# Performance work log

Measured on AMD Instinct MI355X. Metric: run time of the kernel, lower is better.

The kernel has to match this reference:

```python
import jax, jax.numpy as jnp
import numpy as np

NUM_HEADS = 16
HEAD_DIM = 64
WINDOW = 512  # attention_window; band half-width = WINDOW // 2
MAX_TIME = 10000.0  # rotary default max timescale


def apply_rotary(x):
    """Rotary encoding as in pos_encs_lib.apply_rotary_encoding.

    x: [b, t, h, d]. Pairs (x[2i], x[2i+1]) are rotated by angle pos * inv_freq,
    with inv_freq repeated per pair (interleaved layout).
    """
    d = x.shape[-1]
    freq_seq = jnp.arange(d // 2, dtype=jnp.float32) / (d // 2)
    inv_freq = jnp.repeat(MAX_TIME ** -freq_seq, 2)  # [d]
    pos = jnp.arange(x.shape[1], dtype=jnp.float32)
    t = pos[None, :, None, None] * inv_freq[None, None, None, :]  # [1,t,1,d]
    xp = x.reshape(*x.shape[:-1], d // 2, 2)
    x_rot = jnp.stack([-xp[..., 1], xp[..., 0]], axis=-1).reshape(x.shape)
    return x * jnp.cos(t).astype(x.dtype) + x_rot * jnp.sin(t).astype(x.dtype)


def setup_inputs() -> dict:
    key = jax.random.key(0)
    ks = jax.random.split(key, 6)
    B, T, E = 4, 2048, 1024
    H = NUM_HEADS * HEAD_DIM
    return {
        "inputs_q": jax.random.normal(ks[0], (B, T, E), jnp.float32),
        "inputs_kv": jax.random.normal(ks[1], (B, T, E), jnp.float32),
        "Wq": jax.random.normal(ks[2], (E, H), jnp.float32) * 0.02,
        "Wk": jax.random.normal(ks[3], (E, H), jnp.float32) * 0.02,
        "Wv": jax.random.normal(ks[4], (E, H), jnp.float32) * 0.02,
        "Wo": jax.random.normal(ks[5], (H, E), jnp.float32) * 0.02,
    }


def reference(inputs_q, inputs_kv, Wq, Wk, Wv, Wo):
    b, T, E = inputs_q.shape
    q = (inputs_q @ Wq).reshape(b, T, NUM_HEADS, HEAD_DIM)
    k = (inputs_kv @ Wk).reshape(b, T, NUM_HEADS, HEAD_DIM)
    v = (inputs_kv @ Wv).reshape(b, T, NUM_HEADS, HEAD_DIM)
    q = apply_rotary(q)
    k = apply_rotary(k)
    # [b, h, t, T] attention logits, scaled by 1/sqrt(head_dim)
    att = jnp.einsum('bthd,bThd->bhtT', q, k) * (1.0 / np.sqrt(HEAD_DIM))
    # sliding-window band mask: |i - j| <= WINDOW // 2 (matches k-diagonal sum)
    idx = jnp.arange(T)
    band = jnp.abs(idx[:, None] - idx[None, :]) <= (WINDOW // 2)
    att = jnp.where(band, att, jnp.finfo(jnp.float32).min)
    p = jax.nn.softmax(att, axis=-1)
    out = jnp.einsum('bhtT,bThd->bthd', p, v).reshape(b, T, NUM_HEADS * HEAD_DIM)
    return out @ Wo
```

## Files before the change

### kernel.cpp

```cpp
#include <hip/hip_runtime.h>
#include <hip/hip_bf16.h>


typedef __attribute__((ext_vector_type(8))) short s8v;
typedef __attribute__((ext_vector_type(4))) float f4v;

#define MFMA_BF16 __builtin_amdgcn_mfma_f32_16x16x32_bf16

#define ASYNC_CP16(g, l)                                             \
  __builtin_amdgcn_global_load_lds(                                  \
      (const __attribute__((address_space(1))) void*)(g),            \
      (__attribute__((address_space(3))) void*)(l), 16, 0, 0)

#define SWZ(row, g) ((row) * 64 + ((((g) ^ ((row) & 7))) * 8))

__device__ __forceinline__ unsigned short f2bf(float f) {
  union { float f; unsigned int u; } v; v.f = f;
  unsigned int r = (v.u + 0x7fffu + ((v.u >> 16) & 1u)) >> 16;
  return (unsigned short)r;
}

__device__ __forceinline__ unsigned int pack_bf16(float a, float b) {
  union { __hip_bfloat162 h; unsigned int u; } cv;
  cv.h = __float22bfloat162_rn(make_float2(a, b));
  return cv.u;
}

__global__ __launch_bounds__(256) void cvt2_kernel(
    const float* __restrict__ s0, const float* __restrict__ s1,
    unsigned short* __restrict__ d0, unsigned short* __restrict__ d1) {
  int g = blockIdx.x;
  const float* src = (g < 8192) ? s0 : s1;
  unsigned short* dst = (g < 8192) ? d0 : d1;
  int i = ((g & 8191) * 256 + threadIdx.x) * 4;
  float4 v = *(const float4*)(src + i);
  ushort4 o;
  o.x = f2bf(v.x); o.y = f2bf(v.y); o.z = f2bf(v.z); o.w = f2bf(v.w);
  *(ushort4*)(dst + i) = o;
}

__global__ __launch_bounds__(256) void wtrans_kernel(
    const float* __restrict__ W0, const float* __restrict__ W1,
    const float* __restrict__ W2, const float* __restrict__ W3,
    unsigned short* __restrict__ D0, unsigned short* __restrict__ D1,
    unsigned short* __restrict__ D2, unsigned short* __restrict__ D3) {
  const float* W = blockIdx.z == 0 ? W0 : blockIdx.z == 1 ? W1 : blockIdx.z == 2 ? W2 : W3;
  unsigned short* D = blockIdx.z == 0 ? D0 : blockIdx.z == 1 ? D1 : blockIdx.z == 2 ? D2 : D3;
  __shared__ float tile[32][33];
  int n0 = blockIdx.x * 32, k0 = blockIdx.y * 32;
  int tx = threadIdx.x & 31, ty = threadIdx.x >> 5;
#pragma unroll
  for (int r = 0; r < 32; r += 8)
    tile[ty + r][tx] = W[(size_t)(k0 + ty + r) * 1024 + n0 + tx];
  __syncthreads();
#pragma unroll
  for (int r = 0; r < 32; r += 8)
    D[(size_t)(n0 + ty + r) * 1024 + k0 + tx] = f2bf(tile[tx][ty + r]);
}

__global__ __launch_bounds__(256) void proj_gemm(
    const unsigned short* __restrict__ XqBf, const unsigned short* __restrict__ XkvBf,
    const unsigned short* __restrict__ Wtq, const unsigned short* __restrict__ Wtk,
    const unsigned short* __restrict__ Wtv,
    unsigned short* __restrict__ Qb, unsigned short* __restrict__ Kb,
    unsigned short* __restrict__ Vt) {
  const int K = 1024;
  int z = blockIdx.z;
  const unsigned short* A  = (z == 0) ? XqBf : XkvBf;
  const unsigned short* Bt = (z == 0) ? Wtq : (z == 1) ? Wtk : Wtv;

  __shared__ __align__(16) unsigned short sA[128 * 64];
  __shared__ __align__(16) unsigned short sB[128 * 64];

  int tid = threadIdx.x;
  int lane = tid & 63, wave = tid >> 6;
  int quad = lane >> 4, l16 = lane & 15;
  int wm = wave & 1, wn = wave >> 1;
  int m_blk = blockIdx.x * 128, n_blk = blockIdx.y * 128;

  f4v acc[4][4] = {};
  int srow = tid >> 3, sg = (tid & 7) ^ (srow & 7);
  const unsigned short* gA = A + (size_t)(m_blk + srow) * K + sg * 8;
  const unsigned short* gB = Bt + (size_t)(n_blk + srow) * K + sg * 8;

  for (int k0 = 0; k0 < K; k0 += 64) {
#pragma unroll
    for (int i = 0; i < 4; ++i) {
      ASYNC_CP16(gA + (size_t)i * 32 * K + k0, &sA[i * 2048 + tid * 8]);
      ASYNC_CP16(gB + (size_t)i * 32 * K + k0, &sB[i * 2048 + tid * 8]);
    }
    __syncthreads();
#pragma unroll
    for (int ks = 0; ks < 64; ks += 32) {
      s8v af[4], bf[4];
#pragma unroll
      for (int mt = 0; mt < 4; ++mt)
        af[mt] = *(const s8v*)&sA[SWZ(wm * 64 + mt * 16 + l16, quad + (ks >> 3))];
#pragma unroll
      for (int nt = 0; nt < 4; ++nt)
        bf[nt] = *(const s8v*)&sB[SWZ(wn * 64 + nt * 16 + l16, quad + (ks >> 3))];
#pragma unroll
      for (int mt = 0; mt < 4; ++mt)
#pragma unroll
        for (int nt = 0; nt < 4; ++nt)
          acc[mt][nt] = MFMA_BF16(af[mt], bf[nt], acc[mt][nt], 0, 0, 0);
    }
    __syncthreads();
  }

  if (z < 2) {
    unsigned short* Cb = (z == 0) ? Qb : Kb;
    float post = (z == 0) ? 0.125f : 1.0f;
#pragma unroll
    for (int mt = 0; mt < 4; ++mt)
#pragma unroll
      for (int nt = 0; nt < 4; ++nt)
#pragma unroll
        for (int r = 0; r < 4; ++r) {
          int row = m_blk + wm * 64 + mt * 16 + quad * 4 + r;
          int col = n_blk + wn * 64 + nt * 16 + l16;
          float v = acc[mt][nt][r];
          float other = __shfl_xor(v, 1);
          int dh = col & 63;
          int tpos = row & 2047;
          float fi = (float)(dh >> 1) * (1.0f / 32.0f);
          float invf = __expf(-9.210340371976184f * fi);
          float ang = (float)tpos * invf;
          float s, c;
          __sincosf(ang, &s, &c);
          v = (dh & 1) ? (v * c + other * s) : (v * c - other * s);
          Cb[(size_t)row * 1024 + col] = f2bf(v * post);
        }
  } else {
#pragma unroll
    for (int mt = 0; mt < 4; ++mt)
#pragma unroll
      for (int nt = 0; nt < 4; ++nt) {
        int row0 = m_blk + wm * 64 + mt * 16 + quad * 4;
        int col = n_blk + wn * 64 + nt * 16 + l16;
        int bb = row0 >> 11, t = row0 & 2047;
        int hh = col >> 6, dh = col & 63;
        ushort4 pk;
        pk.x = f2bf(acc[mt][nt][0]);
        pk.y = f2bf(acc[mt][nt][1]);
        pk.z = f2bf(acc[mt][nt][2]);
        pk.w = f2bf(acc[mt][nt][3]);
        *(ushort4*)&Vt[(((size_t)bb * 16 + hh) * 64 + dh) * 2048 + t] = pk;
      }
  }
}

__global__ __launch_bounds__(256, 4) void attn_kernel(
    const unsigned short* __restrict__ Qb, const unsigned short* __restrict__ Kb,
    const unsigned short* __restrict__ Vt, unsigned short* __restrict__ Ab) {
  const int T = 2048;
  int t0 = blockIdx.x * 128;
  int h = blockIdx.y, b = blockIdx.z;
  int tid = threadIdx.x, lane = tid & 63, wave = tid >> 6;
  int quad = lane >> 4, l16 = lane & 15;

  __shared__ __align__(16) unsigned short sK[64][72];
  __shared__ __align__(16) unsigned short sV[64][72];
  __shared__ __align__(16) unsigned short sP[4][16][72];

  size_t base = ((size_t)b * T) * 1024 + (size_t)h * 64;
  size_t vbase = ((size_t)b * 16 + h) * 64 * 2048;
  int qlo = t0 + wave * 32;

  s8v bq[2][2];
#pragma unroll
  for (int f = 0; f < 2; ++f) {
    const unsigned short* g = Qb + base + (size_t)(qlo + f * 16 + l16) * 1024;
    bq[f][0] = *(const s8v*)(g + quad * 8);
    bq[f][1] = *(const s8v*)(g + 32 + quad * 8);
  }

  f4v oacc[2][4] = {};
  float mrow[2] = {-1e30f, -1e30f}, lrow[2] = {0.0f, 0.0f};

  int kv_lo = max(0, t0 - 256);
  int kv_hi = min(T, t0 + 128 + 256);
  int ntiles = (kv_hi - kv_lo) >> 6;

  int srow = tid >> 2, sseg = (tid & 3) * 16;
  const unsigned short* gK = Kb + base + (size_t)(kv_lo + srow) * 1024 + sseg;
  const unsigned short* gV = Vt + vbase + (size_t)srow * 2048 + kv_lo + sseg;
  uint4 rk0 = *(const uint4*)gK, rk1 = *(const uint4*)(gK + 8);
  uint4 rv0 = *(const uint4*)gV, rv1 = *(const uint4*)(gV + 8);

  for (int it = 0; it < ntiles; ++it) {
    int kv0 = kv_lo + (it << 6);
    __syncthreads();
    *(uint4*)&sK[srow][sseg] = rk0;
    *(uint4*)&sK[srow][sseg + 8] = rk1;
    *(uint4*)&sV[srow][sseg] = rv0;
    *(uint4*)&sV[srow][sseg + 8] = rv1;
    __syncthreads();
    if (it + 1 < ntiles) {
      const unsigned short* nK = gK + (size_t)(it + 1) * 64 * 1024;
      const unsigned short* nV = gV + (it + 1) * 64;
      rk0 = *(const uint4*)nK; rk1 = *(const uint4*)(nK + 8);
      rv0 = *(const uint4*)nV; rv1 = *(const uint4*)(nV + 8);
    }
    if (kv0 > qlo + 31 + 256 || kv0 + 63 < qlo - 256) continue;

#pragma unroll
    for (int f = 0; f < 2; ++f) {
      int qf = qlo + f * 16;
      int qg = qf + l16;
      f4v sacc[4];
#pragma unroll
      for (int nt = 0; nt < 4; ++nt) {
        s8v ak0 = *(const s8v*)&sK[nt * 16 + l16][quad * 8];
        s8v ak1 = *(const s8v*)&sK[nt * 16 + l16][32 + quad * 8];
        f4v zz = {};
        zz = MFMA_BF16(ak0, bq[f][0], zz, 0, 0, 0);
        sacc[nt] = MFMA_BF16(ak1, bq[f][1], sacc[nt] = zz, 0, 0, 0);
      }
      bool full = (kv0 >= qf - 241) && (kv0 <= qf + 193);
      if (!full) {
#pragma unroll
        for (int nt = 0; nt < 4; ++nt) {
          int kg = kv0 + nt * 16 + quad * 4;
#pragma unroll
          for (int r = 0; r < 4; ++r) {
            int d = qg - (kg + r);
            if (d > 256 || d < -256) sacc[nt][r] = -1e30f;
          }
        }
      }
      float mymax = sacc[0][0];
#pragma unroll
      for (int nt = 0; nt < 4; ++nt)
#pragma unroll
        for (int r = 0; r < 4; ++r) mymax = fmaxf(mymax, sacc[nt][r]);
      mymax = fmaxf(mymax, __shfl_xor(mymax, 16));
      mymax = fmaxf(mymax, __shfl_xor(mymax, 32));

      float mn = fmaxf(mrow[f], mymax);
      float alpha = __expf(mrow[f] - mn);
      mrow[f] = mn;

      float mysum = 0.0f;
#pragma unroll
      for (int nt = 0; nt < 4; ++nt) {
        float e0 = __expf(sacc[nt][0] - mn);
        float e1 = __expf(sacc[nt][1] - mn);
        float e2 = __expf(sacc[nt][2] - mn);
        float e3 = __expf(sacc[nt][3] - mn);
        mysum += (e0 + e1) + (e2 + e3);
        *(uint2*)&sP[wave][l16][nt * 16 + quad * 4] =
            make_uint2(pack_bf16(e0, e1), pack_bf16(e2, e3));
      }
      mysum += __shfl_xor(mysum, 16);
      mysum += __shfl_xor(mysum, 32);
      lrow[f] = lrow[f] * alpha + mysum;

      s8v pb0 = *(const s8v*)&sP[wave][l16][quad * 8];
      s8v pb1 = *(const s8v*)&sP[wave][l16][32 + quad * 8];

#pragma unroll
      for (int dt = 0; dt < 4; ++dt) {
        s8v av0 = *(const s8v*)&sV[dt * 16 + l16][quad * 8];
        s8v av1 = *(const s8v*)&sV[dt * 16 + l16][32 + quad * 8];
        f4v o = oacc[f][dt];
#pragma unroll
        for (int r = 0; r < 4; ++r) o[r] *= alpha;
        o = MFMA_BF16(av0, pb0, o, 0, 0, 0);
        oacc[f][dt] = MFMA_BF16(av1, pb1, o, 0, 0, 0);
      }
    }
  }

#pragma unroll
  for (int f = 0; f < 2; ++f) {
    float inv = 1.0f / lrow[f];
    size_t rowoff = base + (size_t)(qlo + f * 16 + l16) * 1024;
#pragma unroll
    for (int dt = 0; dt < 4; ++dt) {
      float o0 = oacc[f][dt][0] * inv, o1 = oacc[f][dt][1] * inv;
      float o2 = oacc[f][dt][2] * inv, o3 = oacc[f][dt][3] * inv;
      *(uint2*)&Ab[rowoff + dt * 16 + quad * 4] =
          make_uint2(pack_bf16(o0, o1), pack_bf16(o2, o3));
    }
  }
}

__global__ __launch_bounds__(256) void out_gemm(
    const unsigned short* __restrict__ A, const unsigned short* __restrict__ Bt,
    float* __restrict__ C) {
  const int K = 1024;
  __shared__ __align__(16) unsigned short sA[128 * 64];
  __shared__ __align__(16) unsigned short sB[128 * 64];

  int tid = threadIdx.x;
  int lane = tid & 63, wave = tid >> 6;
  int quad = lane >> 4, l16 = lane & 15;
  int wm = wave & 1, wn = wave >> 1;
  int m_blk = blockIdx.x * 128, n_blk = blockIdx.y * 128;

  f4v acc[4][4] = {};
  int srow = tid >> 3, sg = (tid & 7) ^ (srow & 7);
  const unsigned short* gA = A + (size_t)(m_blk + srow) * K + sg * 8;
  const unsigned short* gB = Bt + (size_t)(n_blk + srow) * K + sg * 8;

  for (int k0 = 0; k0 < K; k0 += 64) {
#pragma unroll
    for (int i = 0; i < 4; ++i) {
      ASYNC_CP16(gA + (size_t)i * 32 * K + k0, &sA[i * 2048 + tid * 8]);
      ASYNC_CP16(gB + (size_t)i * 32 * K + k0, &sB[i * 2048 + tid * 8]);
    }
    __syncthreads();
#pragma unroll
    for (int ks = 0; ks < 64; ks += 32) {
      s8v af[4], bf[4];
#pragma unroll
      for (int mt = 0; mt < 4; ++mt)
        af[mt] = *(const s8v*)&sA[SWZ(wm * 64 + mt * 16 + l16, quad + (ks >> 3))];
#pragma unroll
      for (int nt = 0; nt < 4; ++nt)
        bf[nt] = *(const s8v*)&sB[SWZ(wn * 64 + nt * 16 + l16, quad + (ks >> 3))];
#pragma unroll
      for (int mt = 0; mt < 4; ++mt)
#pragma unroll
        for (int nt = 0; nt < 4; ++nt)
          acc[mt][nt] = MFMA_BF16(af[mt], bf[nt], acc[mt][nt], 0, 0, 0);
    }
    __syncthreads();
  }

#pragma unroll
  for (int mt = 0; mt < 4; ++mt)
#pragma unroll
    for (int nt = 0; nt < 4; ++nt)
#pragma unroll
      for (int r = 0; r < 4; ++r) {
        int row = m_blk + wm * 64 + mt * 16 + quad * 4 + r;
        int col = n_blk + wn * 64 + nt * 16 + l16;
        C[(size_t)row * 1024 + col] = acc[mt][nt][r];
      }
}

extern "C" void kernel_launch(void* const* d_in, const int* in_sizes, int n_in,
                              void* d_out, int out_size, void* d_ws, size_t ws_size,
                              hipStream_t stream) {
  const float* Xq  = (const float*)d_in[0];
  const float* Xkv = (const float*)d_in[1];
  const float* Wq  = (const float*)d_in[2];
  const float* Wk  = (const float*)d_in[3];
  const float* Wv  = (const float*)d_in[4];
  const float* Wo  = (const float*)d_in[5];
  float* out = (float*)d_out;

  char* ws = (char*)d_ws;
  const size_t MB = 1ull << 20;
  unsigned short* XqBf  = (unsigned short*)(ws + 0 * MB);
  unsigned short* XkvBf = (unsigned short*)(ws + 16 * MB);
  unsigned short* Wtq   = (unsigned short*)(ws + 32 * MB);
  unsigned short* Wtk   = (unsigned short*)(ws + 34 * MB);
  unsigned short* Wtv   = (unsigned short*)(ws + 36 * MB);
  unsigned short* Wto   = (unsigned short*)(ws + 38 * MB);
  unsigned short* Qb    = (unsigned short*)(ws + 40 * MB);
  unsigned short* Kb    = (unsigned short*)(ws + 56 * MB);
  unsigned short* Vt    = (unsigned short*)(ws + 72 * MB);
  unsigned short* Ab    = XqBf;

  cvt2_kernel<<<16384, 256, 0, stream>>>(Xq, Xkv, XqBf, XkvBf);
  wtrans_kernel<<<dim3(32, 32, 4), 256, 0, stream>>>(Wq, Wk, Wv, Wo, Wtq, Wtk, Wtv, Wto);
  proj_gemm<<<dim3(64, 8, 3), 256, 0, stream>>>(XqBf, XkvBf, Wtq, Wtk, Wtv, Qb, Kb, Vt);
  attn_kernel<<<dim3(16, 16, 4), 256, 0, stream>>>(Qb, Kb, Vt, Ab);
  out_gemm<<<dim3(64, 8), 256, 0, stream>>>(Ab, Wto, out);
}
```

Measured before the change: 259.0 us.

## Merge prep kernels, fuse K/V projections sharing A tile, enlarge attention blocks

Merges the activation conversion and weight transpose into one prep launch. The projection GEMM now computes K and V in the same block, so the shared inputs_kv tile is loaded once and reused for two accumulator sets. The attention kernel now uses 512-thread blocks covering 256 queries, which amortises K/V tile loads over more queries but lowers occupancy. The K/V GEMM blocks do twice the work, which creates load imbalance against the Q blocks and raises register pressure.

```diff
diff --git a/kernel.cpp b/kernel.cpp
--- a/kernel.cpp
+++ b/kernel.cpp
@@ -26,36 +26,39 @@
   return cv.u;
 }
 
-__global__ __launch_bounds__(256) void cvt2_kernel(
+__global__ __launch_bounds__(256) void prep_kernel(
     const float* __restrict__ s0, const float* __restrict__ s1,
-    unsigned short* __restrict__ d0, unsigned short* __restrict__ d1) {
-  int g = blockIdx.x;
-  const float* src = (g < 8192) ? s0 : s1;
-  unsigned short* dst = (g < 8192) ? d0 : d1;
-  int i = ((g & 8191) * 256 + threadIdx.x) * 4;
-  float4 v = *(const float4*)(src + i);
-  ushort4 o;
-  o.x = f2bf(v.x); o.y = f2bf(v.y); o.z = f2bf(v.z); o.w = f2bf(v.w);
-  *(ushort4*)(dst + i) = o;
-}
-
-__global__ __launch_bounds__(256) void wtrans_kernel(
+    unsigned short* __restrict__ d0, unsigned short* __restrict__ d1,
     const float* __restrict__ W0, const float* __restrict__ W1,
     const float* __restrict__ W2, const float* __restrict__ W3,
     unsigned short* __restrict__ D0, unsigned short* __restrict__ D1,
     unsigned short* __restrict__ D2, unsigned short* __restrict__ D3) {
-  const float* W = blockIdx.z == 0 ? W0 : blockIdx.z == 1 ? W1 : blockIdx.z == 2 ? W2 : W3;
-  unsigned short* D = blockIdx.z == 0 ? D0 : blockIdx.z == 1 ? D1 : blockIdx.z == 2 ? D2 : D3;
-  __shared__ float tile[32][33];
-  int n0 = blockIdx.x * 32, k0 = blockIdx.y * 32;
-  int tx = threadIdx.x & 31, ty = threadIdx.x >> 5;
-#pragma unroll
-  for (int r = 0; r < 32; r += 8)
-    tile[ty + r][tx] = W[(size_t)(k0 + ty + r) * 1024 + n0 + tx];
-  __syncthreads();
-#pragma unroll
-  for (int r = 0; r < 32; r += 8)
-    D[(size_t)(n0 + ty + r) * 1024 + k0 + tx] = f2bf(tile[tx][ty + r]);
+  int g = blockIdx.x;
+  if (g < 16384) {
+    const float* src = (g < 8192) ? s0 : s1;
+    unsigned short* dst = (g < 8192) ? d0 : d1;
+    int i = ((g & 8191) * 256 + threadIdx.x) * 4;
+    float4 v = *(const float4*)(src + i);
+    ushort4 o;
+    o.x = f2bf(v.x); o.y = f2bf(v.y); o.z = f2bf(v.z); o.w = f2bf(v.w);
+    *(ushort4*)(dst + i) = o;
+  } else {
+    int w = g - 16384;
+    int z = w >> 10;
+    int rem = w & 1023;
+    const float* W = z == 0 ? W0 : z == 1 ? W1 : z == 2 ? W2 : W3;
+    unsigned short* D = z == 0 ? D0 : z == 1 ? D1 : z == 2 ? D2 : D3;
+    __shared__ float tile[32][33];
+    int n0 = (rem & 31) * 32, k0 = (rem >> 5) * 32;
+    int tx = threadIdx.x & 31, ty = threadIdx.x >> 5;
+#pragma unroll
+    for (int r = 0; r < 32; r += 8)
+      tile[ty + r][tx] = W[(size_t)(k0 + ty + r) * 1024 + n0 + tx];
+    __syncthreads();
+#pragma unroll
+    for (int r = 0; r < 32; r += 8)
+      D[(size_t)(n0 + ty + r) * 1024 + k0 + tx] = f2bf(tile[tx][ty + r]);
+  }
 }
 
 __global__ __launch_bounds__(256) void proj_gemm(
@@ -66,11 +69,12 @@
     unsigned short* __restrict__ Vt) {
   const int K = 1024;
   int z = blockIdx.z;
-  const unsigned short* A  = (z == 0) ? XqBf : XkvBf;
-  const unsigned short* Bt = (z == 0) ? Wtq : (z == 1) ? Wtk : Wtv;
+  const unsigned short* A   = (z == 0) ? XqBf : XkvBf;
+  const unsigned short* Bt0 = (z == 0) ? Wtq : Wtk;
 
   __shared__ __align__(16) unsigned short sA[128 * 64];
-  __shared__ __align__(16) unsigned short sB[128 * 64];
+  __shared__ __align__(16) unsigned short sB0[128 * 64];
+  __shared__ __align__(16) unsigned short sB1[128 * 64];
 
   int tid = threadIdx.x;
   int lane = tid & 63, wave = tid >> 6;
@@ -78,37 +82,55 @@
   int wm = wave & 1, wn = wave >> 1;
   int m_blk = blockIdx.x * 128, n_blk = blockIdx.y * 128;
 
-  f4v acc[4][4] = {};
+  f4v acc0[4][4] = {};
+  f4v acc1[4][4] = {};
   int srow = tid >> 3, sg = (tid & 7) ^ (srow & 7);
-  const unsigned short* gA = A + (size_t)(m_blk + srow) * K + sg * 8;
-  const unsigned short* gB = Bt + (size_t)(n_blk + srow) * K + sg * 8;
+  const unsigned short* gA  = A   + (size_t)(m_blk + srow) * K + sg * 8;
+  const unsigned short* gB0 = Bt0 + (size_t)(n_blk + srow) * K + sg * 8;
+  const unsigned short* gB1 = Wtv + (size_t)(n_blk + srow) * K + sg * 8;
 
   for (int k0 = 0; k0 < K; k0 += 64) {
 #pragma unroll
     for (int i = 0; i < 4; ++i) {
       ASYNC_CP16(gA + (size_t)i * 32 * K + k0, &sA[i * 2048 + tid * 8]);
-      ASYNC_CP16(gB + (size_t)i * 32 * K + k0, &sB[i * 2048 + tid * 8]);
+      ASYNC_CP16(gB0 + (size_t)i * 32 * K + k0, &sB0[i * 2048 + tid * 8]);
+    }
+    if (z == 1) {
+#pragma unroll
+      for (int i = 0; i < 4; ++i)
+        ASYNC_CP16(gB1 + (size_t)i * 32 * K + k0, &sB1[i * 2048 + tid * 8]);
     }
     __syncthreads();
 #pragma unroll
     for (int ks = 0; ks < 64; ks += 32) {
-      s8v af[4], bf[4];
+      s8v af[4], bf0[4];
 #pragma unroll
       for (int mt = 0; mt < 4; ++mt)
         af[mt] = *(const s8v*)&sA[SWZ(wm * 64 + mt * 16 + l16, quad + (ks >> 3))];
 #pragma unroll
       for (int nt = 0; nt < 4; ++nt)
-        bf[nt] = *(const s8v*)&sB[SWZ(wn * 64 + nt * 16 + l16, quad + (ks >> 3))];
+        bf0[nt] = *(const s8v*)&sB0[SWZ(wn * 64 + nt * 16 + l16, quad + (ks >> 3))];
 #pragma unroll
       for (int mt = 0; mt < 4; ++mt)
 #pragma unroll
         for (int nt = 0; nt < 4; ++nt)
-          acc[mt][nt] = MFMA_BF16(af[mt], bf[nt], acc[mt][nt], 0, 0, 0);
-    }
-    __syncthreads();
-  }
-
-  if (z < 2) {
+          acc0[mt][nt] = MFMA_BF16(af[mt], bf0[nt], acc0[mt][nt], 0, 0, 0);
+      if (z == 1) {
+        s8v bf1[4];
+#pragma unroll
+        for (int nt = 0; nt < 4; ++nt)
+          bf1[nt] = *(const s8v*)&sB1[SWZ(wn * 64 + nt * 16 + l16, quad + (ks >> 3))];
+#pragma unroll
+        for (int mt = 0; mt < 4; ++mt)
+#pragma unroll
+          for (int nt = 0; nt < 4; ++nt)
+            acc1[mt][nt] = MFMA_BF16(af[mt], bf1[nt], acc1[mt][nt], 0, 0, 0);
+      }
+    }
+    __syncthreads();
+  }
+
+  {
     unsigned short* Cb = (z == 0) ? Qb : Kb;
     float post = (z == 0) ? 0.125f : 1.0f;
 #pragma unroll
@@ -119,7 +141,7 @@
         for (int r = 0; r < 4; ++r) {
           int row = m_blk + wm * 64 + mt * 16 + quad * 4 + r;
           int col = n_blk + wn * 64 + nt * 16 + l16;
-          float v = acc[mt][nt][r];
+          float v = acc0[mt][nt][r];
           float other = __shfl_xor(v, 1);
           int dh = col & 63;
           int tpos = row & 2047;
@@ -131,7 +153,8 @@
           v = (dh & 1) ? (v * c + other * s) : (v * c - other * s);
           Cb[(size_t)row * 1024 + col] = f2bf(v * post);
         }
-  } else {
+  }
+  if (z == 1) {
 #pragma unroll
     for (int mt = 0; mt < 4; ++mt)
 #pragma unroll
@@ -141,27 +164,27 @@
         int bb = row0 >> 11, t = row0 & 2047;
         int hh = col >> 6, dh = col & 63;
         ushort4 pk;
-        pk.x = f2bf(acc[mt][nt][0]);
-        pk.y = f2bf(acc[mt][nt][1]);
-        pk.z = f2bf(acc[mt][nt][2]);
-        pk.w = f2bf(acc[mt][nt][3]);
+        pk.x = f2bf(acc1[mt][nt][0]);
+        pk.y = f2bf(acc1[mt][nt][1]);
+        pk.z = f2bf(acc1[mt][nt][2]);
+        pk.w = f2bf(acc1[mt][nt][3]);
         *(ushort4*)&Vt[(((size_t)bb * 16 + hh) * 64 + dh) * 2048 + t] = pk;
       }
   }
 }
 
-__global__ __launch_bounds__(256, 4) void attn_kernel(
+__global__ __launch_bounds__(512, 2) void attn_kernel(
     const unsigned short* __restrict__ Qb, const unsigned short* __restrict__ Kb,
     const unsigned short* __restrict__ Vt, unsigned short* __restrict__ Ab) {
   const int T = 2048;
-  int t0 = blockIdx.x * 128;
+  int t0 = blockIdx.x * 256;
   int h = blockIdx.y, b = blockIdx.z;
   int tid = threadIdx.x, lane = tid & 63, wave = tid >> 6;
   int quad = lane >> 4, l16 = lane & 15;
 
   __shared__ __align__(16) unsigned short sK[64][72];
   __shared__ __align__(16) unsigned short sV[64][72];
-  __shared__ __align__(16) unsigned short sP[4][16][72];
+  __shared__ __align__(16) unsigned short sP[8][16][72];
 
   size_t base = ((size_t)b * T) * 1024 + (size_t)h * 64;
   size_t vbase = ((size_t)b * 16 + h) * 64 * 2048;
@@ -179,28 +202,24 @@
   float mrow[2] = {-1e30f, -1e30f}, lrow[2] = {0.0f, 0.0f};
 
   int kv_lo = max(0, t0 - 256);
-  int kv_hi = min(T, t0 + 128 + 256);
+  int kv_hi = min(T, t0 + 256 + 256);
   int ntiles = (kv_hi - kv_lo) >> 6;
 
-  int srow = tid >> 2, sseg = (tid & 3) * 16;
+  int srow = tid >> 3, sseg = (tid & 7) * 8;
   const unsigned short* gK = Kb + base + (size_t)(kv_lo + srow) * 1024 + sseg;
   const unsigned short* gV = Vt + vbase + (size_t)srow * 2048 + kv_lo + sseg;
-  uint4 rk0 = *(const uint4*)gK, rk1 = *(const uint4*)(gK + 8);
-  uint4 rv0 = *(const uint4*)gV, rv1 = *(const uint4*)(gV + 8);
+  uint4 rk = *(const uint4*)gK;
+  uint4 rv = *(const uint4*)gV;
 
   for (int it = 0; it < ntiles; ++it) {
     int kv0 = kv_lo + (it << 6);
     __syncthreads();
-    *(uint4*)&sK[srow][sseg] = rk0;
-    *(uint4*)&sK[srow][sseg + 8] = rk1;
-    *(uint4*)&sV[srow][sseg] = rv0;
-    *(uint4*)&sV[srow][sseg + 8] = rv1;
+    *(uint4*)&sK[srow][sseg] = rk;
+    *(uint4*)&sV[srow][sseg] = rv;
     __syncthreads();
     if (it + 1 < ntiles) {
-      const unsigned short* nK = gK + (size_t)(it + 1) * 64 * 1024;
-      const unsigned short* nV = gV + (it + 1) * 64;
-      rk0 = *(const uint4*)nK; rk1 = *(const uint4*)(nK + 8);
-      rv0 = *(const uint4*)nV; rv1 = *(const uint4*)(nV + 8);
+      rk = *(const uint4*)(gK + (size_t)(it + 1) * 64 * 1024);
+      rv = *(const uint4*)(gV + (it + 1) * 64);
     }
     if (kv0 > qlo + 31 + 256 || kv0 + 63 < qlo - 256) continue;
 
@@ -215,7 +234,7 @@
         s8v ak1 = *(const s8v*)&sK[nt * 16 + l16][32 + quad * 8];
         f4v zz = {};
         zz = MFMA_BF16(ak0, bq[f][0], zz, 0, 0, 0);
-        sacc[nt] = MFMA_BF16(ak1, bq[f][1], sacc[nt] = zz, 0, 0, 0);
+        sacc[nt] = MFMA_BF16(ak1, bq[f][1], zz, 0, 0, 0);
       }
       bool full = (kv0 >= qf - 241) && (kv0 <= qf + 193);
       if (!full) {
@@ -365,9 +384,9 @@
   unsigned short* Vt    = (unsigned short*)(ws + 72 * MB);
   unsigned short* Ab    = XqBf;
 
-  cvt2_kernel<<<16384, 256, 0, stream>>>(Xq, Xkv, XqBf, XkvBf);
-  wtrans_kernel<<<dim3(32, 32, 4), 256, 0, stream>>>(Wq, Wk, Wv, Wo, Wtq, Wtk, Wtv, Wto);
-  proj_gemm<<<dim3(64, 8, 3), 256, 0, stream>>>(XqBf, XkvBf, Wtq, Wtk, Wtv, Qb, Kb, Vt);
-  attn_kernel<<<dim3(16, 16, 4), 256, 0, stream>>>(Qb, Kb, Vt, Ab);
+  prep_kernel<<<20480, 256, 0, stream>>>(Xq, Xkv, XqBf, XkvBf,
+                                         Wq, Wk, Wv, Wo, Wtq, Wtk, Wtv, Wto);
+  proj_gemm<<<dim3(64, 8, 2), 256, 0, stream>>>(XqBf, XkvBf, Wtq, Wtk, Wtv, Qb, Kb, Vt);
+  attn_kernel<<<dim3(8, 16, 4), 512, 0, stream>>>(Qb, Kb, Vt, Ab);
   out_gemm<<<dim3(64, 8), 256, 0, stream>>>(Ab, Wto, out);
 }
```

New measurement: 280.6 us. 1.08x slower.
